# Performance work log

Hardware: AMD Instinct MI355X
Metric: run time of the kernel (lower is better)

The kernel has to match this reference:

```python
import jax, jax.numpy as jnp
import numpy as np
import math

FEATURE_DIM = 512
QK_DIM = 256
EPS = 1e-12  # torch F.normalize eps


def _l2norm(x):
    n = jnp.linalg.norm(x, axis=-1, keepdims=True)
    return x / jnp.maximum(n, EPS)


def setup_inputs() -> dict:
    key = jax.random.key(0)
    ks = jax.random.split(key, 6)
    B, Nq, Nk = 16, 2048, 2048
    query = jax.random.normal(ks[0], (B, Nq, FEATURE_DIM), dtype=jnp.float32)
    key_t = jax.random.normal(ks[1], (B, Nk, FEATURE_DIM // 2), dtype=jnp.float32)
    value = jax.random.normal(ks[2], (B, Nk, FEATURE_DIM // 2), dtype=jnp.float32)
    # weights stored torch-style [out, in], init N(0, sqrt(2/out))
    WQ = jax.random.normal(ks[3], (QK_DIM, FEATURE_DIM), dtype=jnp.float32) * math.sqrt(2.0 / QK_DIM)
    WK = jax.random.normal(ks[4], (QK_DIM, FEATURE_DIM // 2), dtype=jnp.float32) * math.sqrt(2.0 / QK_DIM)
    WV = jax.random.normal(ks[5], (FEATURE_DIM, FEATURE_DIM // 2), dtype=jnp.float32) * math.sqrt(2.0 / FEATURE_DIM)
    return {"query": query, "key": key_t, "value": value, "WQ": WQ, "WK": WK, "WV": WV}


def reference(query, key, value, WQ, WK, WV):
    temp = QK_DIM ** (-0.5)
    w_q = _l2norm(jnp.einsum('bnf,qf->bnq', query, WQ))      # [B, Nq, D]
    w_k = _l2norm(jnp.einsum('bmf,qf->bmq', key, WK))        # [B, Nk, D]
    dot = jnp.einsum('bnd,bmd->bnm', w_q, w_k)               # cosine sims
    affinity = jax.nn.softmax(dot * temp, axis=-1)
    w_v = _l2norm(jnp.einsum('bmf,vf->bmv', value, WV))      # [B, Nk, F]
    out = jnp.einsum('bnm,bmv->bnv', affinity, w_v)
    return out + query
```

## Files before the change

kernel.cpp:

```cpp
#include <hip/hip_runtime.h>

typedef float        f32x4  __attribute__((ext_vector_type(4)));
typedef float        f32x16 __attribute__((ext_vector_type(16)));
typedef unsigned int u32x4  __attribute__((ext_vector_type(4)));
typedef unsigned int u32x2  __attribute__((ext_vector_type(2)));
typedef int          i32x2  __attribute__((ext_vector_type(2)));
typedef __bf16       bf16x8 __attribute__((ext_vector_type(8)));

#define DEVFN static __device__ __forceinline__

DEVFN unsigned cvtpk(float a, float b){
  unsigned r;
  asm("v_cvt_pk_bf16_f32 %0, %1, %2" : "=v"(r) : "v"(a), "v"(b));
  return r;
}
DEVFN float exp2_hw(float x){
  float r;
  asm("v_exp_f32 %0, %1" : "=v"(r) : "v"(x));
  return r;
}
DEVFN bf16x8 as_bf(u32x4 v){ union{u32x4 u; bf16x8 b;} x; x.u=v; return x.b; }

DEVFN unsigned char f2fp8(float v){
  int r = __builtin_amdgcn_cvt_pk_fp8_f32(v, v, 0, false);
  return (unsigned char)(r & 0xff);
}
DEVFN unsigned pk4_fp8(float a, float b, float c, float d){
  int r = __builtin_amdgcn_cvt_pk_fp8_f32(a, b, 0, false);
  r = __builtin_amdgcn_cvt_pk_fp8_f32(c, d, r, true);
  return (unsigned)r;
}
DEVFN long mk64(unsigned lo, unsigned hi){
  return (long)(((unsigned long long)hi << 32) | lo);
}

DEVFN void gload16(const char* src, char* lds){
  __builtin_amdgcn_global_load_lds(
      (__attribute__((address_space(1))) void*)src,
      (__attribute__((address_space(3))) void*)lds, 16, 0, 0);
}

constexpr int BB = 16, NQ = 2048, NK = 2048, F = 512, D = 256, FV = 512;

template<int KD, int ND, int MODE>
DEVFN void proj_body(const float* __restrict__ X, const float* __restrict__ W,
                     unsigned char* __restrict__ Y, float scale,
                     char* sm, float (*wsum)[32], int bid)
{
  constexpr bool TR = (MODE == 2);
  constexpr int NW = ND/4;
  constexpr int AF = TR ? 8 : 2;
  constexpr int BF = TR ? 2 : NW/16;
  constexpr int NIT = KD/32;
  const int tid = threadIdx.x;
  const int lane = tid & 63;
  const int wid = tid >> 6;
  const int q16 = lane & 15;
  const int g = lane >> 4;
  const int row0 = bid * 32;
  const int rX = tid >> 3, cX = (tid & 7) * 4;

  f32x4 z4 = {0.f,0.f,0.f,0.f};
  f32x4 acc[AF][BF];
  #pragma unroll
  for (int i=0;i<AF;i++){
    #pragma unroll
    for (int j=0;j<BF;j++) acc[i][j] = z4;
  }

  f32x4 xr = *(const f32x4*)(X + (size_t)(row0+rX)*KD + cX);
  f32x4 wr[ND/32];
  #pragma unroll
  for (int j=0;j<ND/32;j++)
    wr[j] = *(const f32x4*)(W + (size_t)(j*32+rX)*KD + cX);

  for (int t = 0; t < NIT; ++t){
    char* xb; char* wb;
    if constexpr (TR){ xb = sm; wb = sm + 2560; }
    else { xb = sm + (t&1)*23040; wb = xb + 2560; }
    {
      u32x2 p; p[0]=cvtpk(xr[0],xr[1]); p[1]=cvtpk(xr[2],xr[3]);
      *(u32x2*)(xb + rX*80 + cX*2) = p;
    }
    #pragma unroll
    for (int j=0;j<ND/32;j++){
      u32x2 p; p[0]=cvtpk(wr[j][0],wr[j][1]); p[1]=cvtpk(wr[j][2],wr[j][3]);
      *(u32x2*)(wb + (j*32+rX)*80 + cX*2) = p;
    }
    if (t + 1 < NIT){
      int k0n = (t+1)*32;
      xr = *(const f32x4*)(X + (size_t)(row0+rX)*KD + k0n + cX);
      #pragma unroll
      for (int j=0;j<ND/32;j++)
        wr[j] = *(const f32x4*)(W + (size_t)(j*32+rX)*KD + k0n + cX);
    }
    __syncthreads();
    if constexpr (!TR){
      bf16x8 a[2], bb[BF];
      #pragma unroll
      for (int mi=0;mi<2;mi++)  a[mi]  = as_bf(*(const u32x4*)(xb + (16*mi+q16)*80 + g*16));
      #pragma unroll
      for (int ni=0;ni<BF;ni++) bb[ni] = as_bf(*(const u32x4*)(wb + (wid*NW + 16*ni + q16)*80 + g*16));
      #pragma unroll
      for (int mi=0;mi<2;mi++){
        #pragma unroll
        for (int ni=0;ni<BF;ni++)
          acc[mi][ni] = __builtin_amdgcn_mfma_f32_16x16x32_bf16(a[mi], bb[ni], acc[mi][ni], 0,0,0);
      }
    } else {
      bf16x8 a[8], bb[2];
      #pragma unroll
      for (int ai=0;ai<8;ai++) a[ai] = as_bf(*(const u32x4*)(wb + (wid*NW + 16*ai + q16)*80 + g*16));
      #pragma unroll
      for (int ci=0;ci<2;ci++) bb[ci] = as_bf(*(const u32x4*)(xb + (16*ci+q16)*80 + g*16));
      #pragma unroll
      for (int ai=0;ai<8;ai++){
        #pragma unroll
        for (int ci=0;ci<2;ci++)
          acc[ai][ci] = __builtin_amdgcn_mfma_f32_16x16x32_bf16(a[ai], bb[ci], acc[ai][ci], 0,0,0);
      }
      __syncthreads();
    }
  }

  unsigned char* lds8 = (unsigned char*)sm;

  if constexpr (!TR){
    float part[2][4];
    #pragma unroll
    for (int mi=0;mi<2;mi++){
      #pragma unroll
      for (int r=0;r<4;r++){
        float s=0.f;
        #pragma unroll
        for (int ni=0;ni<BF;ni++){ float v=acc[mi][ni][r]; s += v*v; }
        part[mi][r]=s;
      }
    }
    #pragma unroll
    for (int m=1;m<16;m<<=1){
      #pragma unroll
      for (int mi=0;mi<2;mi++){
        #pragma unroll
        for (int r=0;r<4;r++) part[mi][r] += __shfl_xor(part[mi][r], m);
      }
    }
    __syncthreads();
    if (q16 == 0){
      #pragma unroll
      for (int mi=0;mi<2;mi++){
        #pragma unroll
        for (int r=0;r<4;r++) wsum[wid][16*mi + 4*g + r] = part[mi][r];
      }
    }
    __syncthreads();
    #pragma unroll
    for (int mi=0;mi<2;mi++){
      #pragma unroll
      for (int r=0;r<4;r++){
        int m = 16*mi + 4*g + r;
        float tot = wsum[0][m]+wsum[1][m]+wsum[2][m]+wsum[3][m];
        float inv = scale / fmaxf(sqrtf(tot), 1e-12f);
        #pragma unroll
        for (int ni=0;ni<BF;ni++){
          int col = wid*NW + 16*ni + q16;
          unsigned char vb = f2fp8(acc[mi][ni][r]*inv);
          if constexpr (MODE == 0){
            lds8[m*256 + col] = vb;
          } else {
            int u = col >> 5, dd = col & 31;
            int s = ((dd>>4)<<3) | (dd&7);
            int l = (m & 31) + ((dd>>3)&1)*32;
            lds8[(u*64 + l)*16 + s] = vb;
          }
        }
      }
    }
    __syncthreads();
    unsigned char* dst;
    if constexpr (MODE == 0){
      dst = Y + (size_t)row0*256;
    } else {
      int b2 = row0 >> 11, kt = (row0 & 2047) >> 5;
      dst = Y + (((size_t)b2*64 + kt)*8192);
    }
    #pragma unroll
    for (int pass=0; pass<2; ++pass){
      int off = pass*4096 + tid*16;
      *(u32x4*)(dst + off) = *(const u32x4*)(lds8 + off);
    }
  } else {
    float pp[2];
    #pragma unroll
    for (int ci=0;ci<2;ci++){
      float s=0.f;
      #pragma unroll
      for (int ai=0;ai<8;ai++){
        #pragma unroll
        for (int r=0;r<4;r++){ float v=acc[ai][ci][r]; s += v*v; }
      }
      pp[ci]=s;
    }
    #pragma unroll
    for (int ci=0;ci<2;ci++){
      pp[ci] += __shfl_xor(pp[ci],16);
      pp[ci] += __shfl_xor(pp[ci],32);
    }
    if (lane < 16){ wsum[wid][lane] = pp[0]; wsum[wid][16+lane] = pp[1]; }
    __syncthreads();
    #pragma unroll
    for (int ci=0;ci<2;ci++){
      int m = 16*ci + q16;
      float tot = wsum[0][m]+wsum[1][m]+wsum[2][m]+wsum[3][m];
      float inv = scale / fmaxf(sqrtf(tot), 1e-12f);
      #pragma unroll
      for (int ai=0;ai<8;ai++){
        #pragma unroll
        for (int r=0;r<4;r++){
          int n = wid*NW + 16*ai + 4*g + r;
          int fvb = n >> 5, l31v = n & 31;
          unsigned char vb = f2fp8(acc[ai][ci][r]*inv);
          lds8[(fvb*2 + ci)*512 + l31v*16 + q16] = vb;
        }
      }
    }
    __syncthreads();
    int b2 = row0 >> 11;
    int kvv = row0 & 2047;
    int t64 = kvv >> 6, hh = (kvv >> 5) & 1;
    unsigned char* vbase = Y + ((size_t)b2*32 + t64)*32768;
    #pragma unroll
    for (int pass=0; pass<4; ++pass){
      int L = pass*4096 + tid*16;
      int c = L >> 9, inner = L & 511;
      unsigned char* dst = vbase + (size_t)(c>>1)*2048 + (c&1)*1024 + hh*512 + inner;
      *(u32x4*)dst = *(const u32x4*)(lds8 + L);
    }
  }
}

__global__ __launch_bounds__(256,2) void proj_all(
    const float* __restrict__ query, const float* __restrict__ key,
    const float* __restrict__ value, const float* __restrict__ WQ,
    const float* __restrict__ WK, const float* __restrict__ WV,
    unsigned char* __restrict__ wq8, unsigned char* __restrict__ k8,
    unsigned char* __restrict__ v8, float sq)
{
  __shared__ __align__(16) char sm[46080];
  __shared__ float wsum[4][32];
  const int bid = blockIdx.x;
  if (bid < 1024){
    proj_body<512,256,0>(query, WQ, wq8, sq,   sm, wsum, bid);
  } else if (bid < 2048){
    proj_body<256,256,1>(key,   WK, k8,  8.0f, sm, wsum, bid - 1024);
  } else {
    proj_body<256,512,2>(value, WV, v8,  8.0f, sm, wsum, bid - 2048);
  }
}

__global__ __launch_bounds__(512,2) void attn_kernel(const float* __restrict__ query,
    const unsigned char* __restrict__ wq8, const unsigned char* __restrict__ k8,
    const unsigned char* __restrict__ v8, float* __restrict__ out)
{
  __shared__ __align__(16) char smem[106496];
  const int tid = threadIdx.x, lane = tid & 63, wid = tid >> 6;
  const int l31 = lane & 31, h = lane >> 5;
  const int qs = wid & 3, fvh = wid >> 2;
  const int bid = blockIdx.x;
  const int lb = (bid & 7)*32 + (bid >> 3);
  const int b = lb >> 4;
  const int qblk = lb & 15;
  const int q0 = qblk*128;

  const char* ksrc = (const char*)(k8 + (size_t)b*524288)  + lane*16;
  const char* vsrc = (const char*)(v8 + (size_t)b*1048576) + lane*16;
  char* const pwav = smem + 98304 + qs*2048;

  #define STAGE(T, CUR) do{                                                  \
    gload16(ksrc + (size_t)(T)*16384 + (2*wid  )*1024,                       \
            smem + (CUR)*16384 + (2*wid  )*1024);                            \
    gload16(ksrc + (size_t)(T)*16384 + (2*wid+1)*1024,                       \
            smem + (CUR)*16384 + (2*wid+1)*1024);                            \
    _Pragma("unroll")                                                        \
    for (int i_=0;i_<4;i_++)                                                 \
      gload16(vsrc + (size_t)(T)*32768 + (4*wid+i_)*1024,                    \
              smem + 32768 + (CUR)*32768 + (4*wid+i_)*1024);                 \
  }while(0)

  STAGE(0, 0);

  unsigned long long qf[16];
  {
    const unsigned char* qb = wq8 + ((size_t)b*NQ + q0 + qs*32 + l31)*D;
    #pragma unroll
    for (int c=0;c<16;c++) qf[c] = *(const unsigned long long*)(qb + c*16 + h*8);
  }

  f32x16 z16;
  #pragma unroll
  for (int i=0;i<16;i++) z16[i]=0.f;
  f32x16 o[8];
  #pragma unroll
  for (int i=0;i<8;i++) o[i]=z16;
  float ssum = 0.f;
  const float c2 = 0.0625f * 1.4426950408889634f / 64.0f;

  __syncthreads();

  #define BODY(T, CUR) do{                                                          \
    if ((T) < 31) STAGE((T)+1, (CUR)^1);                                            \
                                         \
    const char* kb = smem + (CUR)*16384 + fvh*8192;                                 \
    f32x16 S = z16;                                                                 \
    __builtin_amdgcn_s_setprio(1);                                                  \
    _Pragma("unroll")                                                               \
    for (int u=0;u<8;u++){                                                          \
      u32x4 kk = *(const u32x4*)(kb + u*1024 + lane*16);                            \
      S = __builtin_amdgcn_mfma_f32_32x32x16_fp8_fp8(mk64(kk[0],kk[1]),             \
            (long)qf[2*u],   S, 0,0,0);                                             \
      S = __builtin_amdgcn_mfma_f32_32x32x16_fp8_fp8(mk64(kk[2],kk[3]),             \
            (long)qf[2*u+1], S, 0,0,0);                                             \
    }                                                                               \
    __builtin_amdgcn_s_setprio(0);                                                  \
    float p[16];                                                                    \
    _Pragma("unroll")                                                               \
    for (int r=0;r<16;r++) p[r] = exp2_hw(S[r]*c2);                                 \
    {                                                                               \
      float s2a = (p[0]+p[1])+(p[2]+p[3]),  s2b = (p[4]+p[5])+(p[6]+p[7]);          \
      float s2c = (p[8]+p[9])+(p[10]+p[11]), s2d = (p[12]+p[13])+(p[14]+p[15]);     \
      ssum += (s2a+s2b) + (s2c+s2d);                                                \
    }                                                                               \
                \
    _Pragma("unroll")                                                               \
    for (int m=0;m<4;m++){                                                          \
      unsigned dw = pk4_fp8(p[4*m],p[4*m+1],p[4*m+2],p[4*m+3]);                     \
      *(unsigned*)(pwav + fvh*1024 + (m*2+h)*128 + l31*4) = dw;                     \
    }                                                                               \
    __syncthreads();                 \
    __builtin_amdgcn_s_setprio(1);                                                  \
    _Pragma("unroll")                                                               \
    for (int s=0;s<2;s++){                                                          \
      unsigned lo0 = *(const unsigned*)(pwav + s*1024 + ((0+h)*2  )*128 + l31*4);   \
      unsigned hi0 = *(const unsigned*)(pwav + s*1024 + ((0+h)*2+1)*128 + l31*4);   \
      unsigned lo1 = *(const unsigned*)(pwav + s*1024 + ((2+h)*2  )*128 + l31*4);   \
      unsigned hi1 = *(const unsigned*)(pwav + s*1024 + ((2+h)*2+1)*128 + l31*4);   \
      long B0 = mk64(lo0, hi0), B1 = mk64(lo1, hi1);                                \
      const char* vb = smem + 32768 + (CUR)*32768 + s*16384 + fvh*8192;             \
      _Pragma("unroll")                                                             \
      for (int u=0;u<8;u++){                                                        \
        u32x4 vv = *(const u32x4*)(vb + u*1024 + lane*16);                          \
        o[u] = __builtin_amdgcn_mfma_f32_32x32x16_fp8_fp8(mk64(vv[0],vv[1]), B0,    \
                                                          o[u], 0,0,0);             \
        o[u] = __builtin_amdgcn_mfma_f32_32x32x16_fp8_fp8(mk64(vv[2],vv[3]), B1,    \
                                                          o[u], 0,0,0);             \
      }                                                                             \
    }                                                                               \
    __builtin_amdgcn_s_setprio(0);                                                  \
    __syncthreads();                   \
  }while(0)

  for (int tt = 0; tt < 32; tt += 2){
    BODY(tt,   0);
    BODY(tt+1, 1);
  }
  #undef BODY
  #undef STAGE

  ssum += __shfl_xor(ssum, 32);
  {
    float* sx = (float*)(smem + 98304);
    sx[(qs*2+fvh)*32 + l31] = ssum;
    __syncthreads();
    ssum += sx[(qs*2+(1-fvh))*32 + l31];
  }
  const float inv = 1.f/(8.f*ssum);
  #pragma unroll
  for (int i=0;i<8;i++){
    #pragma unroll
    for (int r=0;r<16;r++) o[i][r] *= inv;
  }

  char* wsc = smem + qs*16384;
  union U16 { f32x16 v; f32x4 q4[4]; };
  const int swz = (l31 & 7) << 4;
  #pragma unroll
  for (int phase=0; phase<2; ++phase){
    if (fvh == phase){
      #pragma unroll
      for (int hf=0; hf<2; ++hf){
        #pragma unroll
        for (int fc2=0; fc2<4; ++fc2){
          U16 u; u.v = o[hf*4+fc2];
          #pragma unroll
          for (int k=0;k<4;k++){
            *(f32x4*)(wsc + l31*512 + ((fc2*128 + k*32 + h*16) ^ swz)) = u.q4[k];
          }
        }
        #pragma unroll
        for (int p2=0;p2<16;p2++){
          int qr = p2*2 + h;
          f32x4 v = *(const f32x4*)(wsc + qr*512 + ((l31*16) ^ ((qr&7)<<4)));
          size_t row = (size_t)b*NQ + q0 + qs*32 + qr;
          int col = fvh*256 + hf*128 + l31*4;
          f32x4 qv = *(const f32x4*)(query + row*F + col);
          #pragma unroll
          for (int e=0;e<4;e++) v[e] += qv[e];
          *(f32x4*)(out + row*F + col) = v;
        }
      }
    }
    __syncthreads();
  }
}

extern "C" void kernel_launch(void* const* d_in, const int* in_sizes, int n_in,
                              void* d_out, int out_size, void* d_ws, size_t ws_size,
                              hipStream_t stream)
{
  const float* query = (const float*)d_in[0];
  const float* key   = (const float*)d_in[1];
  const float* value = (const float*)d_in[2];
  const float* WQ    = (const float*)d_in[3];
  const float* WK    = (const float*)d_in[4];
  const float* WV    = (const float*)d_in[5];
  float* out = (float*)d_out;

  unsigned char* wq8 = (unsigned char*)d_ws;
  unsigned char* k8  = wq8 + (size_t)BB*NQ*D;
  unsigned char* v8  = k8  + (size_t)BB*NK*D;

  proj_all<<<3072, dim3(256), 0, stream>>>(query, key, value, WQ, WK, WV,
                                           wq8, k8, v8, 8.0f);
  attn_kernel<<<256, dim3(512), 0, stream>>>(query, wq8, k8, v8, out);
}
```

Measured before the change: 157.9 us.

## Stage Q/K projection tiles via async global-to-LDS loads in fp32 with swizzle

For the Q and K projection paths, the register-staged global loads followed by bf16 conversion and LDS stores are replaced with direct global_load_lds copies of fp32 tiles into double-buffered, XOR-swizzled shared memory. The bf16 conversion moves to fragment-load time. This aims to overlap the next tile's fetch with the current MFMA work and to cut VGPR pressure and store instructions. In exchange, LDS usage grows to 72KB, which may reduce occupancy, and each fragment now needs two fp32 LDS reads plus conversion.

Measured after the change: 177.9 us. 12.7% more time.

```diff
diff --git a/kernel.cpp b/kernel.cpp
--- a/kernel.cpp
+++ b/kernel.cpp
@@ -38,6 +38,16 @@
   __builtin_amdgcn_global_load_lds(
       (__attribute__((address_space(1))) void*)src,
       (__attribute__((address_space(3))) void*)lds, 16, 0, 0);
+}
+
+DEVFN bf16x8 ldfrag_f32(const char* base, int rel){
+  int sw = ((rel>>7)&7)<<4;
+  f32x4 f0 = *(const f32x4*)(base + (rel ^ sw));
+  f32x4 f1 = *(const f32x4*)(base + ((rel+16) ^ sw));
+  u32x4 p;
+  p[0]=cvtpk(f0[0],f0[1]); p[1]=cvtpk(f0[2],f0[3]);
+  p[2]=cvtpk(f1[0],f1[1]); p[3]=cvtpk(f1[2],f1[3]);
+  return as_bf(p);
 }
 
 constexpr int BB = 16, NQ = 2048, NK = 2048, F = 512, D = 256, FV = 512;
@@ -68,46 +78,76 @@
     for (int j=0;j<BF;j++) acc[i][j] = z4;
   }
 
-  f32x4 xr = *(const f32x4*)(X + (size_t)(row0+rX)*KD + cX);
-  f32x4 wr[ND/32];
-  #pragma unroll
-  for (int j=0;j<ND/32;j++)
-    wr[j] = *(const f32x4*)(W + (size_t)(j*32+rX)*KD + cX);
-
-  for (int t = 0; t < NIT; ++t){
-    char* xb; char* wb;
-    if constexpr (TR){ xb = sm; wb = sm + 2560; }
-    else { xb = sm + (t&1)*23040; wb = xb + 2560; }
-    {
-      u32x2 p; p[0]=cvtpk(xr[0],xr[1]); p[1]=cvtpk(xr[2],xr[3]);
-      *(u32x2*)(xb + rX*80 + cX*2) = p;
-    }
-    #pragma unroll
-    for (int j=0;j<ND/32;j++){
-      u32x2 p; p[0]=cvtpk(wr[j][0],wr[j][1]); p[1]=cvtpk(wr[j][2],wr[j][3]);
-      *(u32x2*)(wb + (j*32+rX)*80 + cX*2) = p;
-    }
-    if (t + 1 < NIT){
-      int k0n = (t+1)*32;
-      xr = *(const f32x4*)(X + (size_t)(row0+rX)*KD + k0n + cX);
-      #pragma unroll
-      for (int j=0;j<ND/32;j++)
-        wr[j] = *(const f32x4*)(W + (size_t)(j*32+rX)*KD + k0n + cX);
-    }
-    __syncthreads();
-    if constexpr (!TR){
+  if constexpr (!TR){
+    #define STAGE01(T, CUR) do{                                               \
+      char* xb_ = sm + (CUR)*36864;                                           \
+      char* wb_ = xb_ + 4096;                                                 \
+      {                                                                       \
+        int rel = wid*1024 + lane*16;                                         \
+        int ds  = rel ^ (((rel>>7)&7)<<4);                                    \
+        int row = ds>>7, cb = ds & 127;                                       \
+        gload16((const char*)X + ((size_t)(row0+row)*KD + (T)*32)*4 + cb,     \
+                xb_ + rel);                                                   \
+      }                                                                       \
+      _Pragma("unroll")                                                       \
+      for (int j=0;j<8;j++){                                                  \
+        int rel = (wid*8+j)*1024 + lane*16;                                   \
+        int ds  = rel ^ (((rel>>7)&7)<<4);                                    \
+        int row = ds>>7, cb = ds & 127;                                       \
+        gload16((const char*)W + ((size_t)row*KD + (T)*32)*4 + cb,            \
+                wb_ + rel);                                                   \
+      }                                                                       \
+    }while(0)
+
+    STAGE01(0, 0);
+    __syncthreads();
+    for (int t = 0; t < NIT; ++t){
+      const int cur = t & 1;
+      if (t + 1 < NIT) STAGE01(t+1, cur^1);
+      const char* xb = sm + cur*36864;
+      const char* wb = xb + 4096;
       bf16x8 a[2], bb[BF];
       #pragma unroll
-      for (int mi=0;mi<2;mi++)  a[mi]  = as_bf(*(const u32x4*)(xb + (16*mi+q16)*80 + g*16));
-      #pragma unroll
-      for (int ni=0;ni<BF;ni++) bb[ni] = as_bf(*(const u32x4*)(wb + (wid*NW + 16*ni + q16)*80 + g*16));
+      for (int mi=0;mi<2;mi++)
+        a[mi] = ldfrag_f32(xb, (16*mi+q16)*128 + g*32);
+      #pragma unroll
+      for (int ni=0;ni<BF;ni++)
+        bb[ni] = ldfrag_f32(wb, (wid*NW + 16*ni + q16)*128 + g*32);
       #pragma unroll
       for (int mi=0;mi<2;mi++){
         #pragma unroll
         for (int ni=0;ni<BF;ni++)
           acc[mi][ni] = __builtin_amdgcn_mfma_f32_16x16x32_bf16(a[mi], bb[ni], acc[mi][ni], 0,0,0);
       }
-    } else {
+      __syncthreads();
+    }
+    #undef STAGE01
+  } else {
+    f32x4 xr = *(const f32x4*)(X + (size_t)(row0+rX)*KD + cX);
+    f32x4 wr[ND/32];
+    #pragma unroll
+    for (int j=0;j<ND/32;j++)
+      wr[j] = *(const f32x4*)(W + (size_t)(j*32+rX)*KD + cX);
+
+    for (int t = 0; t < NIT; ++t){
+      char* xb = sm; char* wb = sm + 2560;
+      {
+        u32x2 p; p[0]=cvtpk(xr[0],xr[1]); p[1]=cvtpk(xr[2],xr[3]);
+        *(u32x2*)(xb + rX*80 + cX*2) = p;
+      }
+      #pragma unroll
+      for (int j=0;j<ND/32;j++){
+        u32x2 p; p[0]=cvtpk(wr[j][0],wr[j][1]); p[1]=cvtpk(wr[j][2],wr[j][3]);
+        *(u32x2*)(wb + (j*32+rX)*80 + cX*2) = p;
+      }
+      if (t + 1 < NIT){
+        int k0n = (t+1)*32;
+        xr = *(const f32x4*)(X + (size_t)(row0+rX)*KD + k0n + cX);
+        #pragma unroll
+        for (int j=0;j<ND/32;j++)
+          wr[j] = *(const f32x4*)(W + (size_t)(j*32+rX)*KD + k0n + cX);
+      }
+      __syncthreads();
       bf16x8 a[8], bb[2];
       #pragma unroll
       for (int ai=0;ai<8;ai++) a[ai] = as_bf(*(const u32x4*)(wb + (wid*NW + 16*ai + q16)*80 + g*16));
@@ -246,7 +286,7 @@
     unsigned char* __restrict__ wq8, unsigned char* __restrict__ k8,
     unsigned char* __restrict__ v8, float sq)
 {
-  __shared__ __align__(16) char sm[46080];
+  __shared__ __align__(16) char sm[73728];
   __shared__ float wsum[4][32];
   const int bid = blockIdx.x;
   if (bid < 1024){
```
